# Kernel optimization log

Measured on AMD Instinct MI355X. Metric: run time of the kernel, lower is better.

The kernel has to match this reference:

```python
import jax, jax.numpy as jnp
import numpy as np

B, S, D = 2, 2048, 1024
H = 16
HD = D // H  # 64


def _rope_tables(seq_len, head_dim, dtype=jnp.float32):
    inv_freq = 1.0 / (10000.0 ** (jnp.arange(0, head_dim, 2, dtype=jnp.float32) / head_dim))
    t = jnp.arange(seq_len, dtype=jnp.float32)
    freqs = jnp.einsum('i,j->ij', t, inv_freq)            # [S, HD/2]
    emb = jnp.concatenate([freqs, freqs], axis=-1)        # [S, HD]
    return jnp.cos(emb).astype(dtype)[None, None], jnp.sin(emb).astype(dtype)[None, None]


def _rotate_half(x):
    x1, x2 = x[..., : x.shape[-1] // 2], x[..., x.shape[-1] // 2 :]
    return jnp.concatenate([-x2, x1], axis=-1)


def setup_inputs() -> dict:
    key = jax.random.key(0)
    ks = jax.random.split(key, 9)
    s = 0.02
    return {
        'hidden_states': jax.random.normal(ks[0], (B, S, D), jnp.float32),
        'attention_mask': jnp.zeros((B, 1, S, S), jnp.float32),
        'Wq': jax.random.normal(ks[1], (D, D), jnp.float32) * s,
        'bq': jnp.zeros((D,), jnp.float32),
        'Wk': jax.random.normal(ks[2], (D, D), jnp.float32) * s,
        'bk': jnp.zeros((D,), jnp.float32),
        'Wv': jax.random.normal(ks[3], (D, D), jnp.float32) * s,
        'bv': jnp.zeros((D,), jnp.float32),
        'Wo': jax.random.normal(ks[4], (D, D), jnp.float32) * s,
        'bo': jnp.zeros((D,), jnp.float32),
    }


def reference(hidden_states, attention_mask, Wq, bq, Wk, bk, Wv, bv, Wo, bo):
    b, s = hidden_states.shape[:2]
    q = hidden_states @ Wq.T + bq
    k = hidden_states @ Wk.T + bk
    v = hidden_states @ Wv.T + bv
    # [B, H, S, HD]
    q = q.reshape(b, s, H, HD).transpose(0, 2, 1, 3)
    k = k.reshape(b, s, H, HD).transpose(0, 2, 1, 3)
    v = v.reshape(b, s, H, HD).transpose(0, 2, 1, 3)
    cos, sin = _rope_tables(s, HD, q.dtype)
    q = q * cos + _rotate_half(q) * sin
    k = k * cos + _rotate_half(k) * sin
    scaling = HD ** (-0.5)
    scores = jnp.einsum('bhqd,bhkd->bhqk', q, k) * scaling
    scores = scores / jnp.log(jnp.asarray(float(s), scores.dtype))  # dynamic NTK
    scores = scores + attention_mask
    probs = jax.nn.softmax(scores, axis=-1)
    out = jnp.einsum('bhqk,bhkd->bhqd', probs, v)
    out = out.transpose(0, 2, 1, 3).reshape(b, s, H * HD)
    return out @ Wo.T + bo
```

## Files before the change

### kernel.cpp

```cpp
#include <hip/hip_runtime.h>
#include <math.h>

#define S_LEN 2048
#define NHEAD 16
#define HDIM  64

typedef __attribute__((ext_vector_type(8))) short bf16x8;
typedef __attribute__((ext_vector_type(4))) float f32x4;

__device__ __forceinline__ unsigned short f2bf(float f) {
    union { float f; unsigned u; } v; v.f = f;
    unsigned r = v.u + 0x7fffu + ((v.u >> 16) & 1u);
    return (unsigned short)(r >> 16);
}

__device__ __forceinline__ void gl2lds16(const void* g, void* l) {
    __builtin_amdgcn_global_load_lds(
        (__attribute__((address_space(1))) void*)(void*)(g),
        (__attribute__((address_space(3))) void*)(l), 16, 0, 0);
}

__global__ __launch_bounds__(256) void convert_kernel(
    const float* __restrict__ hs, const float* __restrict__ Wq,
    const float* __restrict__ Wk, const float* __restrict__ Wv,
    const float* __restrict__ Wo, unsigned short* __restrict__ dst,
    float2* __restrict__ rtab)
{
    const int bid = blockIdx.x;
    if (bid >= 8192) {
        const int gid = (bid - 8192) * 256 + threadIdx.x;
        const int s = gid >> 5, i = gid & 31;
        const float l2c = 0.41524101186092029f;
        const float freq = exp2f(-(float)i * l2c);
        const float ang = (float)s * freq;
        float2 cs;
        cs.x = cosf(ang);
        cs.y = sinf(ang);
        rtab[gid] = cs;
        return;
    }
    const int gid = bid * 256 + threadIdx.x;
    const int n = gid << 2;
    const float* src; int off;
    if (n < (4 << 20))      { src = hs; off = n; }
    else if (n < (5 << 20)) { src = Wq; off = n - (4 << 20); }
    else if (n < (6 << 20)) { src = Wk; off = n - (5 << 20); }
    else if (n < (7 << 20)) { src = Wv; off = n - (6 << 20); }
    else                    { src = Wo; off = n - (7 << 20); }
    const float4 v = *(const float4*)(src + off);
    ushort4 o;
    o.x = f2bf(v.x); o.y = f2bf(v.y); o.z = f2bf(v.z); o.w = f2bf(v.w);
    *(ushort4*)(dst + n) = o;
}

__global__ __launch_bounds__(256, 3) void qkv_gemm_kernel(
    const unsigned short* __restrict__ X,
    const unsigned short* __restrict__ Wall,
    const float* __restrict__ bq, const float* __restrict__ bk,
    const float* __restrict__ bv, const float2* __restrict__ rtab,
    unsigned short* __restrict__ qo, unsigned short* __restrict__ ko,
    unsigned short* __restrict__ vo)
{
    __shared__ unsigned short As[128 * 64];
    __shared__ unsigned short Bs[128 * 64];

    const int mat = blockIdx.x >> 3;
    const int n0  = (blockIdx.x & 7) << 7;
    const int m0  = blockIdx.y << 7;
    const unsigned short* W = Wall + (mat << 20);
    const float* bias = (mat == 0) ? bq : (mat == 1) ? bk : bv;
    unsigned short* out = (mat == 0) ? qo : (mat == 1) ? ko : vo;

    const int tid = threadIdx.x;
    const int wave = tid >> 6, lane = tid & 63;
    const int quad = lane >> 4, ln = lane & 15;
    const int wm = (wave >> 1) << 6, wn = (wave & 1) << 6;

    const unsigned short* xptr[4];
    const unsigned short* wptr[4];
    #pragma unroll
    for (int L = 0; L < 4; ++L) {
        const int i = tid + (L << 8);
        const int r = i >> 3, cl = i & 7;
        const int cg = (cl ^ (r & 7)) << 3;
        const int rq = r & 63;
        const int tau = (mat < 2)
            ? ((r & 64) | ((rq & 15) << 1) | ((rq >> 4) & 1) | (((rq >> 5) & 1) << 5))
            : ((r & 64) | ((rq & 15) << 2) | (rq >> 4));
        xptr[L] = X + (m0 + r) * 1024 + cg;
        wptr[L] = W + (n0 + tau) * 1024 + cg;
    }

    f32x4 acc[4][4] = {};

    for (int k0 = 0; k0 < 1024; k0 += 64) {
        #pragma unroll
        for (int L = 0; L < 4; ++L) {
            const int i = tid + (L << 8);
            gl2lds16(xptr[L] + k0, &As[i << 3]);
            gl2lds16(wptr[L] + k0, &Bs[i << 3]);
        }
        __syncthreads();
        #pragma unroll
        for (int s = 0; s < 2; ++s) {
            bf16x8 a[4], b[4];
            #pragma unroll
            for (int t = 0; t < 4; ++t) {
                const int ra = wm + (t << 4) + ln;
                a[t] = *(const bf16x8*)&As[(ra << 6) + ((((s << 2) | quad) ^ (ra & 7)) << 3)];
                const int rb = wn + (t << 4) + ln;
                b[t] = *(const bf16x8*)&Bs[(rb << 6) + ((((s << 2) | quad) ^ (rb & 7)) << 3)];
            }
            #pragma unroll
            for (int i = 0; i < 4; ++i)
                #pragma unroll
                for (int j = 0; j < 4; ++j)
                    acc[i][j] = __builtin_amdgcn_mfma_f32_16x16x32_bf16(a[i], b[j], acc[i][j], 0, 0, 0);
        }
        __syncthreads();
    }

    const int h = (n0 + wn) >> 6;

    if (mat < 2) {
        const int nb = n0 + wn + (ln << 1);
        const float b0 = bias[nb],      b1 = bias[nb + 1];
        const float b2 = bias[nb + 32], b3 = bias[nb + 33];
        #pragma unroll
        for (int i = 0; i < 4; ++i) {
            #pragma unroll
            for (int reg = 0; reg < 4; ++reg) {
                const int m = m0 + wm + (i << 4) + (quad << 2) + reg;
                const int b_ = m >> 11, s_ = m & 2047;
                unsigned short* o = out + ((((b_ << 4) + h) << 11) + s_) * 64;
                const float4 cs = *(const float4*)(rtab + (s_ << 5) + (ln << 1));
                const float x1a = acc[i][0][reg] + b0, x1b = acc[i][1][reg] + b1;
                const float x2a = acc[i][2][reg] + b2, x2b = acc[i][3][reg] + b3;
                const float r0a = x1a * cs.x - x2a * cs.y;
                const float r0b = x1b * cs.z - x2b * cs.w;
                const float r1a = x2a * cs.x + x1a * cs.y;
                const float r1b = x2b * cs.z + x1b * cs.w;
                const unsigned ua = __float_as_uint(r0a) + 0x8000u;
                const unsigned ub = __float_as_uint(r0b) + 0x8000u;
                const unsigned uc = __float_as_uint(r1a) + 0x8000u;
                const unsigned ud = __float_as_uint(r1b) + 0x8000u;
                *(unsigned*)(o + (ln << 1))      = __builtin_amdgcn_perm(ub, ua, 0x07060302u);
                *(unsigned*)(o + 32 + (ln << 1)) = __builtin_amdgcn_perm(ud, uc, 0x07060302u);
            }
        }
    } else {
        const float4 bv4 = *(const float4*)(bias + n0 + wn + (ln << 2));
        #pragma unroll
        for (int i = 0; i < 4; ++i)
            #pragma unroll
            for (int reg = 0; reg < 4; ++reg) {
                const int m = m0 + wm + (i << 4) + (quad << 2) + reg;
                const int b_ = m >> 11, s_ = m & 2047;
                unsigned short* o = out + ((((b_ << 4) + h) << 11) + s_) * 64;
                const unsigned ua = __float_as_uint(acc[i][0][reg] + bv4.x) + 0x8000u;
                const unsigned ub = __float_as_uint(acc[i][1][reg] + bv4.y) + 0x8000u;
                const unsigned uc = __float_as_uint(acc[i][2][reg] + bv4.z) + 0x8000u;
                const unsigned ud = __float_as_uint(acc[i][3][reg] + bv4.w) + 0x8000u;
                uint2 w;
                w.x = __builtin_amdgcn_perm(ub, ua, 0x07060302u);
                w.y = __builtin_amdgcn_perm(ud, uc, 0x07060302u);
                *(uint2*)(o + (ln << 2)) = w;
            }
    }
}

__global__ __launch_bounds__(256) void vtrans_kernel(
    const unsigned short* __restrict__ v, unsigned short* __restrict__ vt)
{
    __shared__ unsigned short T[64][66];
    const int bh = blockIdx.x >> 5;
    const int s0 = (blockIdx.x & 31) << 6;
    const int tid = threadIdx.x;
    #pragma unroll
    for (int L = 0; L < 4; ++L) {
        const int i = tid + (L << 8);
        const int r = i >> 4, c4 = (i & 15) << 2;
        const ushort4 in = *(const ushort4*)(v + ((bh << 11) + s0 + r) * 64 + c4);
        T[r][c4 + 0] = in.x; T[r][c4 + 1] = in.y;
        T[r][c4 + 2] = in.z; T[r][c4 + 3] = in.w;
    }
    __syncthreads();
    #pragma unroll
    for (int L = 0; L < 4; ++L) {
        const int i = tid + (L << 8);
        const int hd = i >> 4, c4 = (i & 15) << 2;
        ushort4 o;
        o.x = T[c4 + 0][hd]; o.y = T[c4 + 1][hd];
        o.z = T[c4 + 2][hd]; o.w = T[c4 + 3][hd];
        *(ushort4*)(vt + ((bh << 6) + hd) * 2048 + s0 + c4) = o;
    }
}

__global__ __launch_bounds__(512, 4) void flash_kernel(
    const unsigned short* __restrict__ qb, const unsigned short* __restrict__ kb,
    const unsigned short* __restrict__ vtb, const float* __restrict__ mask,
    unsigned short* __restrict__ attn)
{
    __shared__ unsigned short Ks[2][64 * 64];
    __shared__ unsigned short Vt[2][64 * 64];
    __shared__ unsigned short Ps[8 * 1024];

    const int qt = blockIdx.x & 15;
    const int bh = blockIdx.x >> 4;
    const int b_ = bh >> 4, h = bh & 15;
    const int q0 = qt << 7;

    const int tid = threadIdx.x;
    const int wave = tid >> 6, lane = tid & 63;
    const int quad = lane >> 4, ln = lane & 15;

    const unsigned short* qrow = qb + ((size_t)((bh << 11) + q0 + (wave << 4) + ln) << 6);
    bf16x8 qa0 = *(const bf16x8*)(qrow + (quad << 3));
    bf16x8 qa1 = *(const bf16x8*)(qrow + 32 + (quad << 3));

    const float scale = 0.125f / logf(2048.0f);

    unsigned short* Pw = Ps + (wave << 10);

    int kvo0[4], kvo1[4];
    #pragma unroll
    for (int j = 0; j < 4; ++j) {
        const int r = (j << 4) + ln;
        kvo0[j] = (r << 6) + ((quad ^ (r & 7)) << 3);
        kvo1[j] = kvo0[j] ^ 32;
    }
    int po[4];
    #pragma unroll
    for (int reg = 0; reg < 4; ++reg) {
        const int pr = (quad << 2) + reg;
        po[reg] = (pr << 6) + (((ln >> 1) ^ (pr & 7)) << 3) + ((ln & 1) << 2);
    }
    const int pro0 = (ln << 6) + ((quad ^ (ln & 7)) << 3);
    const int pro1 = pro0 ^ 32;

    const int r0 = tid >> 3, c0 = ((tid & 7) ^ (r0 & 7)) << 3;
    const int p0 = ((r0 & 15) << 2) + (r0 >> 4);
    const unsigned short* kg = kb + ((bh << 11) + p0) * 64 + c0;
    const unsigned short* vg = vtb + ((bh << 6) + r0) * 2048 + c0;
    const float* mptr = mask + ((size_t)b_ << 22)
                      + ((size_t)(q0 + (wave << 4) + (quad << 2)) << 11) + (ln << 2);

    float l_i[4] = {0.f, 0.f, 0.f, 0.f};
    f32x4 O[4] = {};

    gl2lds16(kg, &Ks[0][tid << 3]);
    gl2lds16(vg, &Vt[0][tid << 3]);
    kg += 4096; vg += 64;
    float4 mA[4], mB[4];
    #pragma unroll
    for (int reg = 0; reg < 4; ++reg)
        mA[reg] = *(const float4*)(mptr + (reg << 11));
    mptr += 64;

#define FLASH_STEP(BUF, MR)                                                   \
    {                                                                         \
        f32x4 sacc[4] = {};                                                   \
        {                                                                     \
            bf16x8 bfr[4];                                                    \
            _Pragma("unroll")                                                 \
            for (int j = 0; j < 4; ++j)                                       \
                bfr[j] = *(const bf16x8*)&Ks[BUF][kvo0[j]];                   \
            __builtin_amdgcn_s_setprio(1);                                    \
            _Pragma("unroll")                                                 \
            for (int j = 0; j < 4; ++j)                                       \
                sacc[j] = __builtin_amdgcn_mfma_f32_16x16x32_bf16(            \
                    qa0, bfr[j], sacc[j], 0, 0, 0);                           \
            __builtin_amdgcn_s_setprio(0);                                    \
            _Pragma("unroll")                                                 \
            for (int j = 0; j < 4; ++j)                                       \
                bfr[j] = *(const bf16x8*)&Ks[BUF][kvo1[j]];                   \
            __builtin_amdgcn_s_setprio(1);                                    \
            _Pragma("unroll")                                                 \
            for (int j = 0; j < 4; ++j)                                       \
                sacc[j] = __builtin_amdgcn_mfma_f32_16x16x32_bf16(            \
                    qa1, bfr[j], sacc[j], 0, 0, 0);                           \
            __builtin_amdgcn_s_setprio(0);                                    \
        }                                                                     \
        _Pragma("unroll")                                                     \
        for (int reg = 0; reg < 4; ++reg) {                                   \
            float p0_ = __expf(fmaf(sacc[0][reg], scale, MR[reg].x));         \
            float p1_ = __expf(fmaf(sacc[1][reg], scale, MR[reg].y));         \
            float p2_ = __expf(fmaf(sacc[2][reg], scale, MR[reg].z));         \
            float p3_ = __expf(fmaf(sacc[3][reg], scale, MR[reg].w));         \
            l_i[reg] += (p0_ + p1_) + (p2_ + p3_);                            \
            unsigned u0 = __float_as_uint(p0_) + 0x8000u;                     \
            unsigned u1 = __float_as_uint(p1_) + 0x8000u;                     \
            unsigned u2 = __float_as_uint(p2_) + 0x8000u;                     \
            unsigned u3 = __float_as_uint(p3_) + 0x8000u;                     \
            uint2 w;                                                          \
            w.x = __builtin_amdgcn_perm(u1, u0, 0x07060302u);                 \
            w.y = __builtin_amdgcn_perm(u3, u2, 0x07060302u);                 \
            *(uint2*)&Pw[po[reg]] = w;                                        \
        }                                                                     \
        {                                                                     \
            bf16x8 a_ = *(const bf16x8*)&Pw[pro0];                            \
            bf16x8 bfr[4];                                                    \
            _Pragma("unroll")                                                 \
            for (int j = 0; j < 4; ++j)                                       \
                bfr[j] = *(const bf16x8*)&Vt[BUF][kvo0[j]];                   \
            __builtin_amdgcn_s_setprio(1);                                    \
            _Pragma("unroll")                                                 \
            for (int j = 0; j < 4; ++j)                                       \
                O[j] = __builtin_amdgcn_mfma_f32_16x16x32_bf16(               \
                    a_, bfr[j], O[j], 0, 0, 0);                               \
            __builtin_amdgcn_s_setprio(0);                                    \
            a_ = *(const bf16x8*)&Pw[pro1];                                   \
            _Pragma("unroll")                                                 \
            for (int j = 0; j < 4; ++j)                                       \
                bfr[j] = *(const bf16x8*)&Vt[BUF][kvo1[j]];                   \
            __builtin_amdgcn_s_setprio(1);                                    \
            _Pragma("unroll")                                                 \
            for (int j = 0; j < 4; ++j)                                       \
                O[j] = __builtin_amdgcn_mfma_f32_16x16x32_bf16(               \
                    a_, bfr[j], O[j], 0, 0, 0);                               \
            __builtin_amdgcn_s_setprio(0);                                    \
        }                                                                     \
    }

    for (int it = 0; it < 16; ++it) {
        __syncthreads();
        gl2lds16(kg, &Ks[1][tid << 3]);
        gl2lds16(vg, &Vt[1][tid << 3]);
        kg += 4096; vg += 64;
        #pragma unroll
        for (int reg = 0; reg < 4; ++reg)
            mB[reg] = *(const float4*)(mptr + (reg << 11));
        mptr += 64;

        FLASH_STEP(0, mA)

        __syncthreads();
        if (it < 15) {
            gl2lds16(kg, &Ks[0][tid << 3]);
            gl2lds16(vg, &Vt[0][tid << 3]);
            kg += 4096; vg += 64;
            #pragma unroll
            for (int reg = 0; reg < 4; ++reg)
                mA[reg] = *(const float4*)(mptr + (reg << 11));
            mptr += 64;
        }

        FLASH_STEP(1, mB)
    }
#undef FLASH_STEP

    #pragma unroll
    for (int reg = 0; reg < 4; ++reg) {
        float l = l_i[reg];
        l += __shfl_xor(l, 1);
        l += __shfl_xor(l, 2);
        l += __shfl_xor(l, 4);
        l += __shfl_xor(l, 8);
        const float inv = 1.0f / l;
        const int qr = q0 + (wave << 4) + (quad << 2) + reg;
        unsigned short* op = attn + (((size_t)((b_ << 11) + qr)) << 10) + (h << 6);
        #pragma unroll
        for (int j = 0; j < 4; ++j)
            op[(j << 4) + ln] = f2bf(O[j][reg] * inv);
    }
}

__global__ __launch_bounds__(256, 3) void out_gemm_kernel(
    const unsigned short* __restrict__ X, const unsigned short* __restrict__ W,
    const float* __restrict__ bias, float* __restrict__ out)
{
    __shared__ unsigned short As[128 * 64];
    __shared__ unsigned short Bs[128 * 64];

    const int n0 = blockIdx.x << 7;
    const int m0 = blockIdx.y << 7;
    const int tid = threadIdx.x;
    const int wave = tid >> 6, lane = tid & 63;
    const int quad = lane >> 4, ln = lane & 15;
    const int wm = (wave >> 1) << 6, wn = (wave & 1) << 6;

    const unsigned short* xptr[4];
    const unsigned short* wptr[4];
    #pragma unroll
    for (int L = 0; L < 4; ++L) {
        const int i = tid + (L << 8);
        const int r = i >> 3, cl = i & 7;
        const int cg = (cl ^ (r & 7)) << 3;
        const int rq = r & 63;
        const int tau = (r & 64) | ((rq & 15) << 2) | (rq >> 4);
        xptr[L] = X + (m0 + r) * 1024 + cg;
        wptr[L] = W + (n0 + tau) * 1024 + cg;
    }

    f32x4 acc[4][4] = {};

    for (int k0 = 0; k0 < 1024; k0 += 64) {
        #pragma unroll
        for (int L = 0; L < 4; ++L) {
            const int i = tid + (L << 8);
            gl2lds16(xptr[L] + k0, &As[i << 3]);
            gl2lds16(wptr[L] + k0, &Bs[i << 3]);
        }
        __syncthreads();
        #pragma unroll
        for (int s = 0; s < 2; ++s) {
            bf16x8 a[4], b[4];
            #pragma unroll
            for (int t = 0; t < 4; ++t) {
                const int ra = wm + (t << 4) + ln;
                a[t] = *(const bf16x8*)&As[(ra << 6) + ((((s << 2) | quad) ^ (ra & 7)) << 3)];
                const int rb = wn + (t << 4) + ln;
                b[t] = *(const bf16x8*)&Bs[(rb << 6) + ((((s << 2) | quad) ^ (rb & 7)) << 3)];
            }
            #pragma unroll
            for (int i = 0; i < 4; ++i)
                #pragma unroll
                for (int j = 0; j < 4; ++j)
                    acc[i][j] = __builtin_amdgcn_mfma_f32_16x16x32_bf16(a[i], b[j], acc[i][j], 0, 0, 0);
        }
        __syncthreads();
    }

    const float4 bv4 = *(const float4*)(bias + n0 + wn + (ln << 2));

    #pragma unroll
    for (int i = 0; i < 4; ++i)
        #pragma unroll
        for (int reg = 0; reg < 4; ++reg) {
            const int m = m0 + wm + (i << 4) + (quad << 2) + reg;
            float4 ov;
            ov.x = acc[i][0][reg] + bv4.x;
            ov.y = acc[i][1][reg] + bv4.y;
            ov.z = acc[i][2][reg] + bv4.z;
            ov.w = acc[i][3][reg] + bv4.w;
            *(float4*)(out + m * 1024 + n0 + wn + (ln << 2)) = ov;
        }
}

extern "C" void kernel_launch(void* const* d_in, const int* in_sizes, int n_in,
                              void* d_out, int out_size, void* d_ws, size_t ws_size,
                              hipStream_t stream)
{
    const float* hs   = (const float*)d_in[0];
    const float* mask = (const float*)d_in[1];
    const float* Wq   = (const float*)d_in[2];
    const float* bq   = (const float*)d_in[3];
    const float* Wk   = (const float*)d_in[4];
    const float* bk   = (const float*)d_in[5];
    const float* Wv   = (const float*)d_in[6];
    const float* bv   = (const float*)d_in[7];
    const float* Wo   = (const float*)d_in[8];
    const float* bo   = (const float*)d_in[9];

    unsigned short* ws = (unsigned short*)d_ws;
    const size_t M1 = (size_t)1 << 20;
    unsigned short* hsb   = ws;
    unsigned short* wall  = ws + 4 * M1;
    unsigned short* wob   = ws + 7 * M1;
    unsigned short* qbf   = ws + 8 * M1;
    unsigned short* kbf   = ws + 12 * M1;
    unsigned short* vbf   = ws + 16 * M1;
    unsigned short* vtb   = ws + 20 * M1;
    unsigned short* attnb = ws + 24 * M1;
    float2*         rtab  = (float2*)(ws + 28 * M1);

    convert_kernel<<<8448, 256, 0, stream>>>(hs, Wq, Wk, Wv, Wo, ws, rtab);
    qkv_gemm_kernel<<<dim3(24, 32), 256, 0, stream>>>(hsb, wall, bq, bk, bv, rtab, qbf, kbf, vbf);
    vtrans_kernel<<<1024, 256, 0, stream>>>(vbf, vtb);
    flash_kernel<<<512, 512, 0, stream>>>(qbf, kbf, vtb, mask, attnb);
    out_gemm_kernel<<<dim3(8, 32), 256, 0, stream>>>(attnb, wob, bo, (float*)d_out);
}
```

Baseline: 230.1 us.

## Triple-buffer K/V tiles and software-pipeline QK with softmax/PV across iterations

Moves the flash loop from double to triple LDS buffering for K and V tiles. The QK^T MMA for the next tile is issued before the softmax and PV of the previous tile, so score computation overlaps with exp and PV work. The full __syncthreads is replaced by a manual vmcnt wait plus s_barrier, letting loads stay in flight across iterations. This raises LDS use per block, which may lower occupancy, and depends on the hand-chosen vmcnt counts being correct.

```diff
diff --git a/kernel.cpp b/kernel.cpp
--- a/kernel.cpp
+++ b/kernel.cpp
@@ -201,8 +201,8 @@
     const unsigned short* __restrict__ vtb, const float* __restrict__ mask,
     unsigned short* __restrict__ attn)
 {
-    __shared__ unsigned short Ks[2][64 * 64];
-    __shared__ unsigned short Vt[2][64 * 64];
+    __shared__ unsigned short Ks[3][64 * 64];
+    __shared__ unsigned short Vt[3][64 * 64];
     __shared__ unsigned short Ps[8 * 1024];
 
     const int qt = blockIdx.x & 15;
@@ -247,46 +247,44 @@
 
     float l_i[4] = {0.f, 0.f, 0.f, 0.f};
     f32x4 O[4] = {};
-
-    gl2lds16(kg, &Ks[0][tid << 3]);
-    gl2lds16(vg, &Vt[0][tid << 3]);
-    kg += 4096; vg += 64;
-    float4 mA[4], mB[4];
-    #pragma unroll
-    for (int reg = 0; reg < 4; ++reg)
-        mA[reg] = *(const float4*)(mptr + (reg << 11));
-    mptr += 64;
-
-#define FLASH_STEP(BUF, MR)                                                   \
+    f32x4 S0[4], S1[4];
+    float4 M0[4], M1[4], M2[4];
+
+#define VMEM_PIN() asm volatile("" ::: "memory")
+
+#define QK_STEP(KB, SN)                                                       \
     {                                                                         \
-        f32x4 sacc[4] = {};                                                   \
-        {                                                                     \
-            bf16x8 bfr[4];                                                    \
-            _Pragma("unroll")                                                 \
-            for (int j = 0; j < 4; ++j)                                       \
-                bfr[j] = *(const bf16x8*)&Ks[BUF][kvo0[j]];                   \
-            __builtin_amdgcn_s_setprio(1);                                    \
-            _Pragma("unroll")                                                 \
-            for (int j = 0; j < 4; ++j)                                       \
-                sacc[j] = __builtin_amdgcn_mfma_f32_16x16x32_bf16(            \
-                    qa0, bfr[j], sacc[j], 0, 0, 0);                           \
-            __builtin_amdgcn_s_setprio(0);                                    \
-            _Pragma("unroll")                                                 \
-            for (int j = 0; j < 4; ++j)                                       \
-                bfr[j] = *(const bf16x8*)&Ks[BUF][kvo1[j]];                   \
-            __builtin_amdgcn_s_setprio(1);                                    \
-            _Pragma("unroll")                                                 \
-            for (int j = 0; j < 4; ++j)                                       \
-                sacc[j] = __builtin_amdgcn_mfma_f32_16x16x32_bf16(            \
-                    qa1, bfr[j], sacc[j], 0, 0, 0);                           \
-            __builtin_amdgcn_s_setprio(0);                                    \
-        }                                                                     \
+        _Pragma("unroll")                                                     \
+        for (int j = 0; j < 4; ++j) { f32x4 z_ = {}; SN[j] = z_; }            \
+        bf16x8 bfr[4];                                                        \
+        _Pragma("unroll")                                                     \
+        for (int j = 0; j < 4; ++j)                                           \
+            bfr[j] = *(const bf16x8*)&Ks[KB][kvo0[j]];                        \
+        __builtin_amdgcn_s_setprio(1);                                        \
+        _Pragma("unroll")                                                     \
+        for (int j = 0; j < 4; ++j)                                           \
+            SN[j] = __builtin_amdgcn_mfma_f32_16x16x32_bf16(                  \
+                qa0, bfr[j], SN[j], 0, 0, 0);                                 \
+        __builtin_amdgcn_s_setprio(0);                                        \
+        _Pragma("unroll")                                                     \
+        for (int j = 0; j < 4; ++j)                                           \
+            bfr[j] = *(const bf16x8*)&Ks[KB][kvo1[j]];                        \
+        __builtin_amdgcn_s_setprio(1);                                        \
+        _Pragma("unroll")                                                     \
+        for (int j = 0; j < 4; ++j)                                           \
+            SN[j] = __builtin_amdgcn_mfma_f32_16x16x32_bf16(                  \
+                qa1, bfr[j], SN[j], 0, 0, 0);                                 \
+        __builtin_amdgcn_s_setprio(0);                                        \
+    }
+
+#define FIN_STEP(VB, MC, SP)                                                  \
+    {                                                                         \
         _Pragma("unroll")                                                     \
         for (int reg = 0; reg < 4; ++reg) {                                   \
-            float p0_ = __expf(fmaf(sacc[0][reg], scale, MR[reg].x));         \
-            float p1_ = __expf(fmaf(sacc[1][reg], scale, MR[reg].y));         \
-            float p2_ = __expf(fmaf(sacc[2][reg], scale, MR[reg].z));         \
-            float p3_ = __expf(fmaf(sacc[3][reg], scale, MR[reg].w));         \
+            float p0_ = __expf(fmaf(SP[0][reg], scale, MC[reg].x));           \
+            float p1_ = __expf(fmaf(SP[1][reg], scale, MC[reg].y));           \
+            float p2_ = __expf(fmaf(SP[2][reg], scale, MC[reg].z));           \
+            float p3_ = __expf(fmaf(SP[3][reg], scale, MC[reg].w));           \
             l_i[reg] += (p0_ + p1_) + (p2_ + p3_);                            \
             unsigned u0 = __float_as_uint(p0_) + 0x8000u;                     \
             unsigned u1 = __float_as_uint(p1_) + 0x8000u;                     \
@@ -302,7 +300,7 @@
             bf16x8 bfr[4];                                                    \
             _Pragma("unroll")                                                 \
             for (int j = 0; j < 4; ++j)                                       \
-                bfr[j] = *(const bf16x8*)&Vt[BUF][kvo0[j]];                   \
+                bfr[j] = *(const bf16x8*)&Vt[VB][kvo0[j]];                    \
             __builtin_amdgcn_s_setprio(1);                                    \
             _Pragma("unroll")                                                 \
             for (int j = 0; j < 4; ++j)                                       \
@@ -312,7 +310,7 @@
             a_ = *(const bf16x8*)&Pw[pro1];                                   \
             _Pragma("unroll")                                                 \
             for (int j = 0; j < 4; ++j)                                       \
-                bfr[j] = *(const bf16x8*)&Vt[BUF][kvo1[j]];                   \
+                bfr[j] = *(const bf16x8*)&Vt[VB][kvo1[j]];                    \
             __builtin_amdgcn_s_setprio(1);                                    \
             _Pragma("unroll")                                                 \
             for (int j = 0; j < 4; ++j)                                       \
@@ -322,32 +320,56 @@
         }                                                                     \
     }
 
-    for (int it = 0; it < 16; ++it) {
-        __syncthreads();
-        gl2lds16(kg, &Ks[1][tid << 3]);
-        gl2lds16(vg, &Vt[1][tid << 3]);
-        kg += 4096; vg += 64;
-        #pragma unroll
-        for (int reg = 0; reg < 4; ++reg)
-            mB[reg] = *(const float4*)(mptr + (reg << 11));
-        mptr += 64;
-
-        FLASH_STEP(0, mA)
-
-        __syncthreads();
-        if (it < 15) {
-            gl2lds16(kg, &Ks[0][tid << 3]);
-            gl2lds16(vg, &Vt[0][tid << 3]);
-            kg += 4096; vg += 64;
-            #pragma unroll
-            for (int reg = 0; reg < 4; ++reg)
-                mA[reg] = *(const float4*)(mptr + (reg << 11));
-            mptr += 64;
-        }
-
-        FLASH_STEP(1, mB)
-    }
-#undef FLASH_STEP
+#define ITER(KB, VB, WB, MW, MC, SN, SP, DOSTAGE)                             \
+    {                                                                         \
+        asm volatile("s_waitcnt vmcnt(4)" ::: "memory");                      \
+        __builtin_amdgcn_s_barrier();                                         \
+        if (DOSTAGE) {                                                        \
+            gl2lds16(kg, &Ks[WB][tid << 3]);                                  \
+            gl2lds16(vg, &Vt[WB][tid << 3]);                                  \
+            VMEM_PIN();                                                       \
+            kg += 4096; vg += 64;                                             \
+        }                                                                     \
+        _Pragma("unroll")                                                     \
+        for (int reg = 0; reg < 4; ++reg)                                     \
+            MW[reg] = *(const float4*)(mptr + (reg << 11));                   \
+        mptr += 64;                                                           \
+        QK_STEP(KB, SN)                                                       \
+        FIN_STEP(VB, MC, SP)                                                  \
+    }
+
+    gl2lds16(kg, &Ks[0][tid << 3]);
+    gl2lds16(vg, &Vt[0][tid << 3]);
+    VMEM_PIN();
+    kg += 4096; vg += 64;
+    gl2lds16(kg, &Ks[1][tid << 3]);
+    gl2lds16(vg, &Vt[1][tid << 3]);
+    VMEM_PIN();
+    kg += 4096; vg += 64;
+    #pragma unroll
+    for (int reg = 0; reg < 4; ++reg)
+        M0[reg] = *(const float4*)(mptr + (reg << 11));
+    mptr += 64;
+    asm volatile("s_waitcnt vmcnt(6)" ::: "memory");
+    __builtin_amdgcn_s_barrier();
+    QK_STEP(0, S0)
+
+    #pragma unroll 1
+    for (int t = 0; t < 5; ++t) {
+        ITER(1, 0, 2, M1, M0, S1, S0, 1)
+        ITER(2, 1, 0, M2, M1, S0, S1, 1)
+        ITER(0, 2, 1, M0, M2, S1, S0, 1)
+        ITER(1, 0, 2, M1, M0, S0, S1, 1)
+        ITER(2, 1, 0, M2, M1, S1, S0, 1)
+        ITER(0, 2, 1, M0, M2, S0, S1, 1)
+    }
+    ITER(1, 0, 2, M1, M0, S1, S0, 0)
+    FIN_STEP(1, M1, S1)
+
+#undef ITER
+#undef FIN_STEP
+#undef QK_STEP
+#undef VMEM_PIN
 
     #pragma unroll
     for (int reg = 0; reg < 4; ++reg) {
```

New measurement: 416.5 us. 1.81x slower.
